# Optimization experiments

Hardware: AMD Instinct MI355X
Metric: run time of the kernel (lower is better)

## Reference

```python
import jax, jax.numpy as jnp
import numpy as np

DT = 1e-3   # time step [s] (geometry.dt)
H = 10.0    # grid spacing [m] (geometry.h)

# Staggered-grid first differences (2nd-order accurate on the staggered grid).
# Periodic wrap at the boundary via roll; the damping layer d absorbs there.

def _dplus(f, ax):
    return (jnp.roll(f, -1, axis=ax) - f) / H

def _dminus(f, ax):
    return (f - jnp.roll(f, 1, axis=ax)) / H


def setup_inputs() -> dict:
    key = jax.random.key(0)
    ks = jax.random.split(key, 9)
    B, NZ, NX = 4, 2048, 2048
    vp = 1500.0 + 2500.0 * jax.random.uniform(ks[0], (NZ, NX), jnp.float32)   # P velocity [m/s]
    vs = vp / 1.73                                                            # S velocity (Poisson solid)
    rho = 1000.0 + 1000.0 * jax.random.uniform(ks[1], (NZ, NX), jnp.float32)  # density [kg/m^3]
    fields = {}
    for i, name in enumerate(['vx', 'vz', 'txx', 'tzz', 'txz']):
        fields[name] = 1e-3 * jax.random.normal(ks[2 + i], (B, NZ, NX), jnp.float32)
    d = 50.0 * jax.random.uniform(ks[8], (NZ, NX), jnp.float32)               # PML damping profile
    return dict(vp=vp, vs=vs, rho=rho, **fields, d=d)


def reference(vp, vs, rho, vx, vz, txx, tzz, txz, d):
    # Lame parameters from (vp, vs, rho)
    mu = rho * vs * vs
    lam = rho * vp * vp - 2.0 * mu
    # Split-free damping update: y = (1-c)/(1+c) * y_old + dt/(1+c) * rhs
    c = 0.5 * DT * d            # [nz, nx], broadcasts over shot dim
    a = (1.0 - c) / (1.0 + c)
    b = DT / (1.0 + c)
    # --- velocity update (leapfrog: uses old stresses) ---
    vx_new = a * vx + b * (_dminus(txx, -1) + _dminus(txz, -2)) / rho
    vz_new = a * vz + b * (_dplus(txz, -1) + _dplus(tzz, -2)) / rho
    # --- stress update (uses new velocities) ---
    vx_x = _dplus(vx_new, -1)
    vz_z = _dminus(vz_new, -2)
    txx_new = a * txx + b * ((lam + 2.0 * mu) * vx_x + lam * vz_z)
    tzz_new = a * tzz + b * ((lam + 2.0 * mu) * vz_z + lam * vx_x)
    txz_new = a * txz + b * mu * (_dplus(vx_new, -2) + _dminus(vz_new, -1))
    # hidden state for next time step: [5, B, nz, nx]
    return jnp.stack([vx_new, vz_new, txx_new, tzz_new, txz_new])
```

## Files before the change

### kernel.cpp

```cpp
#include <hip/hip_runtime.h>


constexpr int NZ = 2048;
constexpr int NX = 2048;
constexpr int B  = 4;
constexpr int PLANE = NZ * NX;
constexpr int VOL   = B * PLANE;
constexpr float DT    = 1e-3f;
constexpr float INV_H = 0.1f;

constexpr int ZB   = 8;
constexpr int XR   = 128;
constexpr int NROW = ZB + 2;
constexpr int RF4  = 34;
constexpr int ROWF = 140;
constexpr int F4PF = NROW * RF4;
constexpr int TOT  = 5 * F4PF;
constexpr int NBLK = PLANE / (ZB * XR);
constexpr int NXCD = 8;
constexpr int BLK_PER_XCD = NBLK / NXCD;

typedef float f32x4 __attribute__((ext_vector_type(4)));

__device__ __forceinline__ float rcpf(float x) { return __builtin_amdgcn_rcpf(x); }
__device__ __forceinline__ float4 ld4(const float* __restrict__ p) {
    return *reinterpret_cast<const float4*>(p);
}
__device__ __forceinline__ void st4(float* __restrict__ p,
                                    float a, float b, float c, float d) {
    f32x4 v = {a, b, c, d};
    *reinterpret_cast<f32x4*>(p) = v;
}

__global__ __launch_bounds__(256) void wave_fused_v13(
    const float* __restrict__ vp,  const float* __restrict__ vs,
    const float* __restrict__ rho,
    const float* __restrict__ vx,  const float* __restrict__ vz,
    const float* __restrict__ txx, const float* __restrict__ tzz,
    const float* __restrict__ txz,
    const float* __restrict__ dd,
    float* __restrict__ out)
{
    __shared__ float lds[5 * NROW * ROWF];

    const int bid = blockIdx.x;
    const int sb  = (bid & (NXCD - 1)) * BLK_PER_XCD + (bid >> 3);
    const int tz  = sb >> 4;
    const int tx  = sb & 15;
    const int z0  = tz << 3;
    const int x0  = tx << 7;
    const int tid = threadIdx.x;
    const int xt  = tid & 31;
    const int zt  = tid >> 5;

    const int z   = z0 + zt;
    const int x   = x0 + (xt << 2);
    const int zp  = (z + 1) & (NZ - 1);
    const int zm  = (z - 1) & (NZ - 1);
    const int xm1 = (x - 1) & (NX - 1);
    const int xp4 = (x + 4) & (NX - 1);
    const int rz  = z  * NX;
    const int rzp = zp * NX;
    const int rzm = zm * NX;

    const float* sp[7];
    int dst7[7];
    {
        #pragma unroll
        for (int k = 0; k < 7; ++k) {
            const int idx = k * 256 + tid;
            const int f   = idx / F4PF;
            const int rem = idx - f * F4PF;
            const int rr  = rem / RF4;
            const int c   = rem - rr * RF4;
            const int gz  = (z0 - 1 + rr) & (NZ - 1);
            const int gx  = (x0 - 4 + (c << 2)) & (NX - 1);
            const float* fp = (f == 0) ? txx : (f == 1) ? txz
                            : (f == 2) ? tzz : (f == 3) ? vx
                            : (f == 4) ? vz  : txx;
            sp[k]   = fp + gz * NX + gx;
            dst7[k] = (f * NROW + rr) * ROWF + (c << 2);
        }
    }
    const bool act6 = tid < (TOT - 6 * 256);

    float dz6[6], rz6[6];
    {
        const float4 d4 = ld4(dd + rz + x);
        dz6[0] = dd[rz + xm1]; dz6[1] = d4.x; dz6[2] = d4.y;
        dz6[3] = d4.z;         dz6[4] = d4.w; dz6[5] = dd[rz + xp4];
        const float4 r4 = ld4(rho + rz + x);
        rz6[0] = rho[rz + xm1]; rz6[1] = r4.x; rz6[2] = r4.y;
        rz6[3] = r4.z;          rz6[4] = r4.w; rz6[5] = rho[rz + xp4];
    }
    float avz[6], bvz[6], inv_c[4];
    #pragma unroll
    for (int j = 0; j < 6; ++j) {
        const float c   = 0.5f * DT * dz6[j];
        const float inv = rcpf(1.0f + c);
        avz[j] = (1.0f - c) * inv;
        bvz[j] = DT * INV_H * inv * rcpf(rz6[j]);
        if (j >= 1 && j <= 4) inv_c[j - 1] = inv;
    }
    float avzp[4], bvzp[4], avzm[4], bvzm[4];
    {
        const float4 dp = ld4(dd + rzp + x), dm = ld4(dd + rzm + x);
        const float4 rp = ld4(rho + rzp + x), rm = ld4(rho + rzm + x);
        const float dpa[4] = {dp.x, dp.y, dp.z, dp.w};
        const float dma[4] = {dm.x, dm.y, dm.z, dm.w};
        const float rpa[4] = {rp.x, rp.y, rp.z, rp.w};
        const float rma[4] = {rm.x, rm.y, rm.z, rm.w};
        #pragma unroll
        for (int k = 0; k < 4; ++k) {
            float c = 0.5f * DT * dpa[k];
            float inv = rcpf(1.0f + c);
            avzp[k] = (1.0f - c) * inv;
            bvzp[k] = DT * INV_H * inv * rcpf(rpa[k]);
            c = 0.5f * DT * dma[k];
            inv = rcpf(1.0f + c);
            avzm[k] = (1.0f - c) * inv;
            bvzm[k] = DT * INV_H * inv * rcpf(rma[k]);
        }
    }
    float q1[4], q2[4], q3[4];
    {
        const float4 vp4 = ld4(vp + rz + x), vs4 = ld4(vs + rz + x);
        const float vpa[4] = {vp4.x, vp4.y, vp4.z, vp4.w};
        const float vsa[4] = {vs4.x, vs4.y, vs4.z, vs4.w};
        #pragma unroll
        for (int k = 0; k < 4; ++k) {
            const float r   = rz6[k + 1];
            const float muv = r * vsa[k] * vsa[k];
            const float lam = r * vpa[k] * vpa[k] - 2.0f * muv;
            const float bsH = DT * INV_H * inv_c[k];
            q1[k] = bsH * (lam + 2.0f * muv);
            q2[k] = bsH * lam;
            q3[k] = bsH * muv;
        }
    }

    const int lx   = 4 + (xt << 2);
    const int rowT = (0 * NROW + zt) * ROWF + lx;
    const int rowX = (1 * NROW + zt) * ROWF + lx;
    const int rowZ = (2 * NROW + zt) * ROWF + lx;
    const int rowV = (3 * NROW + zt) * ROWF + lx;
    const int rowW = (4 * NROW + zt) * ROWF + lx;
    auto L4 = [&](int off) -> f32x4 {
        return *reinterpret_cast<const f32x4*>(&lds[off]);
    };

    f32x4 sv[7];
    #pragma unroll
    for (int k = 0; k < 7; ++k)
        sv[k] = *reinterpret_cast<const f32x4*>(sp[k]);

    #pragma unroll 1
    for (int b = 0; b < B; ++b) {
        if (b) __syncthreads();

        #pragma unroll
        for (int k = 0; k < 6; ++k)
            *reinterpret_cast<f32x4*>(&lds[dst7[k]]) = sv[k];
        if (act6)
            *reinterpret_cast<f32x4*>(&lds[dst7[6]]) = sv[6];
        __syncthreads();

        if (b < B - 1) {
            const int nb3 = (b + 1) * PLANE;
            #pragma unroll
            for (int k = 0; k < 7; ++k)
                sv[k] = *reinterpret_cast<const f32x4*>(sp[k] + nb3);
        }

        float txxz[6], txzz[6], tzzz[5], tzzzp[5], txxzp[5];
        float txzzm[5], vxz[5], vzz[5];
        float txzzp4[4], tzzzm4[4], vxzp4[4], vzzm4[4];
        {
            f32x4 m, e;
            m = L4(rowT + ROWF);      e = L4(rowT + ROWF - 4);
            txxz[1] = m.x; txxz[2] = m.y; txxz[3] = m.z; txxz[4] = m.w;
            txxz[0] = e.w;            e = L4(rowT + ROWF + 4);
            txxz[5] = e.x;
            m = L4(rowX + ROWF);      e = L4(rowX + ROWF - 4);
            txzz[1] = m.x; txzz[2] = m.y; txzz[3] = m.z; txzz[4] = m.w;
            txzz[0] = e.w;            e = L4(rowX + ROWF + 4);
            txzz[5] = e.x;
            m = L4(rowZ + ROWF);      e = L4(rowZ + ROWF - 4);
            tzzz[1] = m.x; tzzz[2] = m.y; tzzz[3] = m.z; tzzz[4] = m.w;
            tzzz[0] = e.w;
            m = L4(rowZ + 2 * ROWF);  e = L4(rowZ + 2 * ROWF - 4);
            tzzzp[1] = m.x; tzzzp[2] = m.y; tzzzp[3] = m.z; tzzzp[4] = m.w;
            tzzzp[0] = e.w;
            m = L4(rowT + 2 * ROWF);  e = L4(rowT + 2 * ROWF - 4);
            txxzp[1] = m.x; txxzp[2] = m.y; txxzp[3] = m.z; txxzp[4] = m.w;
            txxzp[0] = e.w;
            m = L4(rowX);             e = L4(rowX + 4);
            txzzm[0] = m.x; txzzm[1] = m.y; txzzm[2] = m.z; txzzm[3] = m.w;
            txzzm[4] = e.x;
            m = L4(rowV + ROWF);      e = L4(rowV + ROWF + 4);
            vxz[0] = m.x; vxz[1] = m.y; vxz[2] = m.z; vxz[3] = m.w;
            vxz[4] = e.x;
            m = L4(rowW + ROWF);      e = L4(rowW + ROWF - 4);
            vzz[1] = m.x; vzz[2] = m.y; vzz[3] = m.z; vzz[4] = m.w;
            vzz[0] = e.w;
            m = L4(rowX + 2 * ROWF);
            txzzp4[0] = m.x; txzzp4[1] = m.y; txzzp4[2] = m.z; txzzp4[3] = m.w;
            m = L4(rowZ);
            tzzzm4[0] = m.x; tzzzm4[1] = m.y; tzzzm4[2] = m.z; tzzzm4[3] = m.w;
            m = L4(rowV + 2 * ROWF);
            vxzp4[0] = m.x; vxzp4[1] = m.y; vxzp4[2] = m.z; vxzp4[3] = m.w;
            m = L4(rowW);
            vzzm4[0] = m.x; vzzm4[1] = m.y; vzzm4[2] = m.z; vzzm4[3] = m.w;
        }

        float vxn_z[5];
        #pragma unroll
        for (int k = 0; k < 5; ++k)
            vxn_z[k] = avz[k + 1] * vxz[k]
                     + bvz[k + 1] * ((txxz[k + 1] - txxz[k])
                                   + (txzz[k + 1] - txzzm[k]));
        float vzn_z[5];
        #pragma unroll
        for (int k = 0; k < 5; ++k)
            vzn_z[k] = avz[k] * vzz[k]
                     + bvz[k] * ((txzz[k + 1] - txzz[k])
                               + (tzzzp[k] - tzzz[k]));
        float vxn_zp[4];
        #pragma unroll
        for (int k = 0; k < 4; ++k)
            vxn_zp[k] = avzp[k] * vxzp4[k]
                      + bvzp[k] * ((txxzp[k + 1] - txxzp[k])
                                 + (txzzp4[k] - txzz[k + 1]));
        float vzn_zm[4];
        #pragma unroll
        for (int k = 0; k < 4; ++k)
            vzn_zm[k] = avzm[k] * vzzm4[k]
                      + bvzm[k] * ((txzzm[k + 1] - txzzm[k])
                                 + (tzzz[k + 1] - tzzzm4[k]));

        float oxx[4], ozz[4], oxz[4];
        #pragma unroll
        for (int k = 0; k < 4; ++k) {
            const float dvx = vxn_z[k + 1] - vxn_z[k];
            const float dvz = vzn_z[k + 1] - vzn_zm[k];
            oxx[k] = avz[k + 1] * txxz[k + 1] + q1[k] * dvx + q2[k] * dvz;
            ozz[k] = avz[k + 1] * tzzz[k + 1] + q1[k] * dvz + q2[k] * dvx;
            oxz[k] = avz[k + 1] * txzz[k + 1]
                   + q3[k] * ((vxn_zp[k] - vxn_z[k])
                            + (vzn_z[k + 1] - vzn_z[k]));
        }

        const int cz = b * PLANE + rz + x;
        st4(out + 0 * VOL + cz, vxn_z[0], vxn_z[1], vxn_z[2], vxn_z[3]);
        st4(out + 1 * VOL + cz, vzn_z[1], vzn_z[2], vzn_z[3], vzn_z[4]);
        st4(out + 2 * VOL + cz, oxx[0], oxx[1], oxx[2], oxx[3]);
        st4(out + 3 * VOL + cz, ozz[0], ozz[1], ozz[2], ozz[3]);
        st4(out + 4 * VOL + cz, oxz[0], oxz[1], oxz[2], oxz[3]);
    }
}

extern "C" void kernel_launch(void* const* d_in, const int* in_sizes, int n_in,
                              void* d_out, int out_size, void* d_ws, size_t ws_size,
                              hipStream_t stream) {
    const float* vp  = (const float*)d_in[0];
    const float* vs  = (const float*)d_in[1];
    const float* rho = (const float*)d_in[2];
    const float* vx  = (const float*)d_in[3];
    const float* vz  = (const float*)d_in[4];
    const float* txx = (const float*)d_in[5];
    const float* tzz = (const float*)d_in[6];
    const float* txz = (const float*)d_in[7];
    const float* dd  = (const float*)d_in[8];
    float* out = (float*)d_out;

    const int threads = 256;
    const int blocks  = NBLK;
    hipLaunchKernelGGL(wave_fused_v13, dim3(blocks), dim3(threads), 0, stream,
                       vp, vs, rho, vx, vz, txx, tzz, txz, dd, out);
}
```

Measured before the change: 591.0 us.

## Double-buffer shared-memory tiles across the shot loop with one barrier per iteration

Shared memory is split into two halves. The first shot's tile is written before the loop, and each iteration writes the next shot's tile into the other half while computing from the current one. Global prefetch now runs two shots ahead, and the two barriers per iteration become one. This costs twice the shared memory (about 56 KB per block), which may lower occupancy on a kernel that is mostly memory-bandwidth bound.

```diff
diff --git a/kernel.cpp b/kernel.cpp
--- a/kernel.cpp
+++ b/kernel.cpp
@@ -16,6 +16,7 @@
 constexpr int ROWF = 140;
 constexpr int F4PF = NROW * RF4;
 constexpr int TOT  = 5 * F4PF;
+constexpr int BUF  = 5 * NROW * ROWF;
 constexpr int NBLK = PLANE / (ZB * XR);
 constexpr int NXCD = 8;
 constexpr int BLK_PER_XCD = NBLK / NXCD;
@@ -32,7 +33,7 @@
     *reinterpret_cast<f32x4*>(p) = v;
 }
 
-__global__ __launch_bounds__(256) void wave_fused_v13(
+__global__ __launch_bounds__(256) void wave_fused_v14(
     const float* __restrict__ vp,  const float* __restrict__ vs,
     const float* __restrict__ rho,
     const float* __restrict__ vx,  const float* __restrict__ vz,
@@ -41,7 +42,7 @@
     const float* __restrict__ dd,
     float* __restrict__ out)
 {
-    __shared__ float lds[5 * NROW * ROWF];
+    __shared__ float lds[2 * BUF];
 
     const int bid = blockIdx.x;
     const int sb  = (bid & (NXCD - 1)) * BLK_PER_XCD + (bid >> 3);
@@ -153,20 +154,30 @@
     #pragma unroll
     for (int k = 0; k < 7; ++k)
         sv[k] = *reinterpret_cast<const f32x4*>(sp[k]);
+    #pragma unroll
+    for (int k = 0; k < 6; ++k)
+        *reinterpret_cast<f32x4*>(&lds[dst7[k]]) = sv[k];
+    if (act6)
+        *reinterpret_cast<f32x4*>(&lds[dst7[6]]) = sv[6];
+    #pragma unroll
+    for (int k = 0; k < 7; ++k)
+        sv[k] = *reinterpret_cast<const f32x4*>(sp[k] + PLANE);
+    __syncthreads();
 
     #pragma unroll 1
     for (int b = 0; b < B; ++b) {
-        if (b) __syncthreads();
-
-        #pragma unroll
-        for (int k = 0; k < 6; ++k)
-            *reinterpret_cast<f32x4*>(&lds[dst7[k]]) = sv[k];
-        if (act6)
-            *reinterpret_cast<f32x4*>(&lds[dst7[6]]) = sv[6];
-        __syncthreads();
+        const int cbase = (b & 1) * BUF;
 
         if (b < B - 1) {
-            const int nb3 = (b + 1) * PLANE;
+            const int woff = ((b + 1) & 1) * BUF;
+            #pragma unroll
+            for (int k = 0; k < 6; ++k)
+                *reinterpret_cast<f32x4*>(&lds[woff + dst7[k]]) = sv[k];
+            if (act6)
+                *reinterpret_cast<f32x4*>(&lds[woff + dst7[6]]) = sv[6];
+        }
+        if (b < B - 2) {
+            const int nb3 = (b + 2) * PLANE;
             #pragma unroll
             for (int k = 0; k < 7; ++k)
                 sv[k] = *reinterpret_cast<const f32x4*>(sp[k] + nb3);
@@ -177,39 +188,39 @@
         float txzzp4[4], tzzzm4[4], vxzp4[4], vzzm4[4];
         {
             f32x4 m, e;
-            m = L4(rowT + ROWF);      e = L4(rowT + ROWF - 4);
+            m = L4(cbase + rowT + ROWF);      e = L4(cbase + rowT + ROWF - 4);
             txxz[1] = m.x; txxz[2] = m.y; txxz[3] = m.z; txxz[4] = m.w;
-            txxz[0] = e.w;            e = L4(rowT + ROWF + 4);
+            txxz[0] = e.w;            e = L4(cbase + rowT + ROWF + 4);
             txxz[5] = e.x;
-            m = L4(rowX + ROWF);      e = L4(rowX + ROWF - 4);
+            m = L4(cbase + rowX + ROWF);      e = L4(cbase + rowX + ROWF - 4);
             txzz[1] = m.x; txzz[2] = m.y; txzz[3] = m.z; txzz[4] = m.w;
-            txzz[0] = e.w;            e = L4(rowX + ROWF + 4);
+            txzz[0] = e.w;            e = L4(cbase + rowX + ROWF + 4);
             txzz[5] = e.x;
-            m = L4(rowZ + ROWF);      e = L4(rowZ + ROWF - 4);
+            m = L4(cbase + rowZ + ROWF);      e = L4(cbase + rowZ + ROWF - 4);
             tzzz[1] = m.x; tzzz[2] = m.y; tzzz[3] = m.z; tzzz[4] = m.w;
             tzzz[0] = e.w;
-            m = L4(rowZ + 2 * ROWF);  e = L4(rowZ + 2 * ROWF - 4);
+            m = L4(cbase + rowZ + 2 * ROWF);  e = L4(cbase + rowZ + 2 * ROWF - 4);
             tzzzp[1] = m.x; tzzzp[2] = m.y; tzzzp[3] = m.z; tzzzp[4] = m.w;
             tzzzp[0] = e.w;
-            m = L4(rowT + 2 * ROWF);  e = L4(rowT + 2 * ROWF - 4);
+            m = L4(cbase + rowT + 2 * ROWF);  e = L4(cbase + rowT + 2 * ROWF - 4);
             txxzp[1] = m.x; txxzp[2] = m.y; txxzp[3] = m.z; txxzp[4] = m.w;
             txxzp[0] = e.w;
-            m = L4(rowX);             e = L4(rowX + 4);
+            m = L4(cbase + rowX);             e = L4(cbase + rowX + 4);
             txzzm[0] = m.x; txzzm[1] = m.y; txzzm[2] = m.z; txzzm[3] = m.w;
             txzzm[4] = e.x;
-            m = L4(rowV + ROWF);      e = L4(rowV + ROWF + 4);
+            m = L4(cbase + rowV + ROWF);      e = L4(cbase + rowV + ROWF + 4);
             vxz[0] = m.x; vxz[1] = m.y; vxz[2] = m.z; vxz[3] = m.w;
             vxz[4] = e.x;
-            m = L4(rowW + ROWF);      e = L4(rowW + ROWF - 4);
+            m = L4(cbase + rowW + ROWF);      e = L4(cbase + rowW + ROWF - 4);
             vzz[1] = m.x; vzz[2] = m.y; vzz[3] = m.z; vzz[4] = m.w;
             vzz[0] = e.w;
-            m = L4(rowX + 2 * ROWF);
+            m = L4(cbase + rowX + 2 * ROWF);
             txzzp4[0] = m.x; txzzp4[1] = m.y; txzzp4[2] = m.z; txzzp4[3] = m.w;
-            m = L4(rowZ);
+            m = L4(cbase + rowZ);
             tzzzm4[0] = m.x; tzzzm4[1] = m.y; tzzzm4[2] = m.z; tzzzm4[3] = m.w;
-            m = L4(rowV + 2 * ROWF);
+            m = L4(cbase + rowV + 2 * ROWF);
             vxzp4[0] = m.x; vxzp4[1] = m.y; vxzp4[2] = m.z; vxzp4[3] = m.w;
-            m = L4(rowW);
+            m = L4(cbase + rowW);
             vzzm4[0] = m.x; vzzm4[1] = m.y; vzzm4[2] = m.z; vzzm4[3] = m.w;
         }
 
@@ -256,6 +267,8 @@
         st4(out + 2 * VOL + cz, oxx[0], oxx[1], oxx[2], oxx[3]);
         st4(out + 3 * VOL + cz, ozz[0], ozz[1], ozz[2], ozz[3]);
         st4(out + 4 * VOL + cz, oxz[0], oxz[1], oxz[2], oxz[3]);
+
+        if (b < B - 1) __syncthreads();
     }
 }
 
@@ -275,6 +288,6 @@
 
     const int threads = 256;
     const int blocks  = NBLK;
-    hipLaunchKernelGGL(wave_fused_v13, dim3(blocks), dim3(threads), 0, stream,
+    hipLaunchKernelGGL(wave_fused_v14, dim3(blocks), dim3(threads), 0, stream,
                        vp, vs, rho, vx, vz, txx, tzz, txz, dd, out);
 }
```

Result: no change. 597.5 us (+1.1%).
